# Kernel optimization log

Hardware: AMD Instinct MI355X
Metric: run time of the kernel (lower is better)

## Reference

```python
import jax, jax.numpy as jnp
import numpy as np

N = 200000
D = 256
B = 512  # fixed num_segments (batch.max()+1 in the torch code)
LN_EPS = 1e-5


def _layernorm(h, gamma, beta):
    mu = jnp.mean(h, axis=-1, keepdims=True)
    var = jnp.var(h, axis=-1, keepdims=True)
    return (h - mu) * jax.lax.rsqrt(var + LN_EPS) * gamma + beta


def setup_inputs() -> dict:
    key = jax.random.key(0)
    ks = jax.random.split(key, 10)
    x = jax.random.normal(ks[0], (N, D), dtype=jnp.float32)
    batch = jnp.sort(jax.random.randint(ks[1], (N,), 0, B)).astype(jnp.int64)
    s = 0.05
    return {
        "x": x,
        "batch": batch,
        "vn_embed": jax.random.normal(ks[2], (1, D), dtype=jnp.float32) * 0.02,
        "W1": jax.random.normal(ks[3], (D, D), dtype=jnp.float32) * s,
        "b1": jnp.zeros((D,), dtype=jnp.float32),
        "g1": jnp.ones((D,), dtype=jnp.float32),
        "be1": jnp.zeros((D,), dtype=jnp.float32),
        "W2": jax.random.normal(ks[4], (D, D), dtype=jnp.float32) * s,
        "b2": jnp.zeros((D,), dtype=jnp.float32),
        "g2": jnp.ones((D,), dtype=jnp.float32),
        "be2": jnp.zeros((D,), dtype=jnp.float32),
        "Wg": jax.random.normal(ks[5], (2 * D, D), dtype=jnp.float32) * s,
        "bg": jnp.zeros((D,), dtype=jnp.float32),
    }


def reference(x, batch, vn_embed, W1, b1, g1, be1, W2, b2, g2, be2, Wg, bg):
    # scatter-mean: per-graph average of node features  [B, D]
    seg_sum = jax.ops.segment_sum(x, batch, num_segments=B)
    cnt = jax.ops.segment_sum(jnp.ones((x.shape[0],), x.dtype), batch, num_segments=B)
    node_agg = seg_sum / jnp.maximum(cnt, 1.0)[:, None]
    # node_to_vn: Linear + GELU(exact) + LayerNorm (dropout = identity at eval)
    vn_update = _layernorm(jax.nn.gelu(node_agg @ W1 + b1, approximate=False), g1, be1)
    vn_state = vn_embed + vn_update  # vn_embed broadcasts [1,D] -> [B,D]
    # gather broadcast back to nodes + vn_to_node MLP
    vn_broadcast = vn_state[batch]  # [N, D]
    node_update = _layernorm(jax.nn.gelu(vn_broadcast @ W2 + b2, approximate=False), g2, be2)
    # sigmoid gate on concat + gated residual
    gate = jax.nn.sigmoid(jnp.concatenate([x, node_update], axis=-1) @ Wg + bg)
    x_out = x + gate * node_update
    return (x_out, vn_state)
```

## Files before the change

kernel.cpp:

```cpp
#include <hip/hip_runtime.h>
#include <hip/hip_bf16.h>
#include <math.h>

#define DIM 256
#define B_SEG 512
#define LN_EPS 1e-5f

typedef __attribute__((ext_vector_type(8))) short bf16x8;
typedef __attribute__((ext_vector_type(4))) float f32x4;

__device__ __forceinline__ float gelu_exact(float v) {
    return 0.5f * v * (1.0f + erff(v * 0.70710678118654752f));
}

__device__ __forceinline__ unsigned int pack2bf(float a, float b) {
    unsigned int ua = (unsigned int)__bfloat16_as_ushort(__float2bfloat16(a));
    unsigned int ub = (unsigned int)__bfloat16_as_ushort(__float2bfloat16(b));
    return ua | (ub << 16);
}

__device__ __forceinline__ void async16(const void* g, void* l) {
    __builtin_amdgcn_global_load_lds(
        (const __attribute__((address_space(1))) void*)(g),
        (__attribute__((address_space(3))) void*)(l), 16, 0, 0);
}

__global__ __launch_bounds__(256) void k_wprep(const float* __restrict__ Wg,
                                               __hip_bfloat16* __restrict__ Wt2) {
    int k = blockIdx.x;
    int c = threadIdx.x;
    Wt2[((size_t)(k >> 3) << 11) + (c << 3) + (k & 7)] = __float2bfloat16(Wg[(size_t)k * DIM + c]);
}

__global__ __launch_bounds__(256) void k_bounds(const int* __restrict__ batch,
                                                int* __restrict__ seg_start, int n) {
    int s = blockIdx.x * 256 + threadIdx.x;
    if (s > B_SEG) return;
    int lo = 0, hi = n;
    while (lo < hi) {
        int mid = (lo + hi) >> 1;
        if (batch[mid] < s) lo = mid + 1; else hi = mid;
    }
    seg_start[s] = lo;
}

__global__ __launch_bounds__(256) void k_segsum2(const float* __restrict__ x,
                                                 const int* __restrict__ seg_start,
                                                 float* __restrict__ partial,
                                                 __hip_bfloat16* __restrict__ xbf,
                                                 int emit) {
    const int seg  = blockIdx.x >> 1;
    const int half = blockIdx.x & 1;
    const int s0 = seg_start[seg], s1 = seg_start[seg + 1];
    const int hl = (s1 - s0 + 1) >> 1;
    const int rs = s0 + half * hl;
    const int re = half ? s1 : (s0 + hl);

    const int wave = threadIdx.x >> 6;
    const int lane = threadIdx.x & 63;
    const int dby  = lane * 8;

    float4 acc = make_float4(0.f, 0.f, 0.f, 0.f);

    for (int r0 = rs; r0 < re; r0 += 16) {
        float4 v[4];
        #pragma unroll
        for (int jj = 0; jj < 4; ++jj) {
            int r = r0 + 4 * jj + wave;
            v[jj] = (r < re) ? *(const float4*)(x + (size_t)r * DIM + lane * 4)
                             : make_float4(0.f, 0.f, 0.f, 0.f);
        }
        __builtin_amdgcn_sched_barrier(0);
        #pragma unroll
        for (int jj = 0; jj < 4; ++jj) {
            int r = r0 + 4 * jj + wave;
            if (r < re) {
                if (emit) {
                    uint2 pk;
                    pk.x = pack2bf(v[jj].x, v[jj].y);
                    pk.y = pack2bf(v[jj].z, v[jj].w);
                    *(uint2*)((char*)xbf + (size_t)r * 512 + (dby ^ ((r & 7) << 4))) = pk;
                }
                acc.x += v[jj].x; acc.y += v[jj].y; acc.z += v[jj].z; acc.w += v[jj].w;
            }
        }
    }

    __shared__ float4 red[4][64];
    red[wave][lane] = acc;
    __syncthreads();
    if (wave == 0) {
        float4 a0 = red[0][lane], a1 = red[1][lane], a2 = red[2][lane], a3 = red[3][lane];
        float4 t;
        t.x = (a0.x + a1.x) + (a2.x + a3.x);
        t.y = (a0.y + a1.y) + (a2.y + a3.y);
        t.z = (a0.z + a1.z) + (a2.z + a3.z);
        t.w = (a0.w + a1.w) + (a2.w + a3.w);
        *(float4*)(partial + ((size_t)half * B_SEG + seg) * DIM + lane * 4) = t;
    }
}

__global__ __launch_bounds__(256) void k_vn(const float* __restrict__ partial,
                                            const int* __restrict__ seg_start,
                                            const float* __restrict__ vn_embed,
                                            const float* __restrict__ W1, const float* __restrict__ b1,
                                            const float* __restrict__ g1, const float* __restrict__ be1,
                                            const float* __restrict__ W2, const float* __restrict__ b2,
                                            const float* __restrict__ g2, const float* __restrict__ be2,
                                            const float* __restrict__ Wg, const float* __restrict__ bg,
                                            float* __restrict__ vn_state_out,
                                            float* __restrict__ nu,
                                            float* __restrict__ gpart) {
    __shared__ float sIn[DIM];
    __shared__ float sRed[DIM];
    __shared__ float sRed2[DIM];
    const int b = blockIdx.x;
    const int d = threadIdx.x;

    float cntf = (float)(seg_start[b + 1] - seg_start[b]);
    float denom = fmaxf(cntf, 1.0f);
    sIn[d] = (partial[(size_t)b * DIM + d] +
              partial[(size_t)(B_SEG + b) * DIM + d]) / denom;
    __syncthreads();

    float h0 = 0.f, h1 = 0.f, h2a = 0.f, h3 = 0.f;
    for (int k = 0; k < DIM; k += 4) {
        h0  = fmaf(sIn[k + 0], W1[(size_t)(k + 0) * DIM + d], h0);
        h1  = fmaf(sIn[k + 1], W1[(size_t)(k + 1) * DIM + d], h1);
        h2a = fmaf(sIn[k + 2], W1[(size_t)(k + 2) * DIM + d], h2a);
        h3  = fmaf(sIn[k + 3], W1[(size_t)(k + 3) * DIM + d], h3);
    }
    float h = gelu_exact(b1[d] + ((h0 + h1) + (h2a + h3)));

    sRed[d] = h; sRed2[d] = h * h;
    __syncthreads();
    for (int s = 128; s > 0; s >>= 1) {
        if (d < s) { sRed[d] += sRed[d + s]; sRed2[d] += sRed2[d + s]; }
        __syncthreads();
    }
    float mu = sRed[0] * (1.0f / DIM);
    float var = fmaxf(sRed2[0] * (1.0f / DIM) - mu * mu, 0.0f);
    float rs = rsqrtf(var + LN_EPS);
    float vnst = vn_embed[d] + ((h - mu) * rs * g1[d] + be1[d]);
    vn_state_out[(size_t)b * DIM + d] = vnst;
    __syncthreads();
    sIn[d] = vnst;
    __syncthreads();

    float g0 = 0.f, g1a = 0.f, g2a = 0.f, g3 = 0.f;
    for (int k = 0; k < DIM; k += 4) {
        g0  = fmaf(sIn[k + 0], W2[(size_t)(k + 0) * DIM + d], g0);
        g1a = fmaf(sIn[k + 1], W2[(size_t)(k + 1) * DIM + d], g1a);
        g2a = fmaf(sIn[k + 2], W2[(size_t)(k + 2) * DIM + d], g2a);
        g3  = fmaf(sIn[k + 3], W2[(size_t)(k + 3) * DIM + d], g3);
    }
    float h2 = gelu_exact(b2[d] + ((g0 + g1a) + (g2a + g3)));

    sRed[d] = h2; sRed2[d] = h2 * h2;
    __syncthreads();
    for (int s = 128; s > 0; s >>= 1) {
        if (d < s) { sRed[d] += sRed[d + s]; sRed2[d] += sRed2[d + s]; }
        __syncthreads();
    }
    float mu2 = sRed[0] * (1.0f / DIM);
    float var2 = fmaxf(sRed2[0] * (1.0f / DIM) - mu2 * mu2, 0.0f);
    float rs2 = rsqrtf(var2 + LN_EPS);
    float nud = (h2 - mu2) * rs2 * g2[d] + be2[d];
    nu[(size_t)b * DIM + d] = nud;
    __syncthreads();
    sIn[d] = nud;
    __syncthreads();

    float p0 = 0.f, p1 = 0.f, p2 = 0.f, p3 = 0.f;
    for (int k = 0; k < DIM; k += 4) {
        p0 = fmaf(sIn[k + 0], Wg[(size_t)(DIM + k + 0) * DIM + d], p0);
        p1 = fmaf(sIn[k + 1], Wg[(size_t)(DIM + k + 1) * DIM + d], p1);
        p2 = fmaf(sIn[k + 2], Wg[(size_t)(DIM + k + 2) * DIM + d], p2);
        p3 = fmaf(sIn[k + 3], Wg[(size_t)(DIM + k + 3) * DIM + d], p3);
    }
    gpart[(size_t)b * DIM + d] = bg[d] + ((p0 + p1) + (p2 + p3));
}

__global__ __launch_bounds__(256, 4) void k_gate_bf(const __hip_bfloat16* __restrict__ xbf,
                                                    const int* __restrict__ batch,
                                                    const __hip_bfloat16* __restrict__ Wt2,
                                                    const float* __restrict__ nu,
                                                    const float* __restrict__ gpart,
                                                    float* __restrict__ xout,
                                                    int n) {
    __shared__ __align__(16) char sA[64 * 512];

    const int tid  = threadIdx.x;
    const int wave = tid >> 6;
    const int lane = tid & 63;
    const int r15  = lane & 15;
    const int kq   = lane >> 4;
    const size_t i0 = (size_t)blockIdx.x * 64;

    const char* gsrc = (const char*)xbf + i0 * 512;
    #pragma unroll
    for (int j = 0; j < 8; ++j)
        async16(gsrc + j * 4096 + tid * 16, sA + j * 4096 + wave * 1024);
    __syncthreads();

    f32x4 acc[4][4];
    #pragma unroll
    for (int m = 0; m < 4; ++m)
        #pragma unroll
        for (int nn = 0; nn < 4; ++nn)
            acc[m][nn] = (f32x4){0.f, 0.f, 0.f, 0.f};

    #pragma unroll
    for (int ks = 0; ks < 8; ++ks) {
        bf16x8 a[4], b[4];
        #pragma unroll
        for (int nn = 0; nn < 4; ++nn) {
            int c = wave * 64 + nn * 16 + r15;
            b[nn] = *(const bf16x8*)(Wt2 + ((size_t)(ks * 4 + kq) << 11) + (c << 3));
        }
        #pragma unroll
        for (int m = 0; m < 4; ++m) {
            int r = m * 16 + r15;
            a[m] = *(const bf16x8*)(sA + r * 512 + ((ks * 64 + kq * 16) ^ ((r & 7) << 4)));
        }
        #pragma unroll
        for (int m = 0; m < 4; ++m)
            #pragma unroll
            for (int nn = 0; nn < 4; ++nn)
                acc[m][nn] = __builtin_amdgcn_mfma_f32_16x16x32_bf16(a[m], b[nn], acc[m][nn], 0, 0, 0);
    }

    #pragma unroll
    for (int m = 0; m < 4; ++m) {
        #pragma unroll
        for (int q = 0; q < 4; ++q) {
            int rr = m * 16 + kq * 4 + q;
            long node = (long)(i0 + rr);
            if (node >= n) continue;
            int bb = batch[node];
            #pragma unroll
            for (int nn = 0; nn < 4; ++nn) {
                int col = wave * 64 + nn * 16 + r15;
                float pre = acc[m][nn][q] + gpart[bb * DIM + col];
                float e = __expf(-pre);
                float gte = __builtin_amdgcn_rcpf(1.0f + e);
                float xres = __bfloat162float(
                    *(const __hip_bfloat16*)(sA + rr * 512 + ((2 * col) ^ ((rr & 7) << 4))));
                xout[(size_t)node * DIM + col] = xres + gte * nu[bb * DIM + col];
            }
        }
    }
}

__global__ __launch_bounds__(256) void k_segsum_fp(const float* __restrict__ x,
                                                   const int* __restrict__ batch,
                                                   float* __restrict__ sums,
                                                   int n) {
    const int i0 = blockIdx.x * 64;
    if (i0 >= n) return;
    const int t    = threadIdx.x;
    const int lane = t & 63;
    const int d4   = lane * 4;
    const int rg   = t >> 6;
    float4 acc = make_float4(0.f, 0.f, 0.f, 0.f);
    int cur = -1;
    for (int j = 0; j < 16; ++j) {
        int i = i0 + rg + 4 * j;
        if (i >= n) break;
        int b = batch[i];
        if (b != cur) {
            if (cur >= 0) {
                atomicAdd(&sums[(size_t)cur * DIM + d4 + 0], acc.x);
                atomicAdd(&sums[(size_t)cur * DIM + d4 + 1], acc.y);
                atomicAdd(&sums[(size_t)cur * DIM + d4 + 2], acc.z);
                atomicAdd(&sums[(size_t)cur * DIM + d4 + 3], acc.w);
            }
            acc = make_float4(0.f, 0.f, 0.f, 0.f);
            cur = b;
        }
        float4 v = *(const float4*)(x + (size_t)i * DIM + d4);
        acc.x += v.x; acc.y += v.y; acc.z += v.z; acc.w += v.w;
    }
    if (cur >= 0) {
        atomicAdd(&sums[(size_t)cur * DIM + d4 + 0], acc.x);
        atomicAdd(&sums[(size_t)cur * DIM + d4 + 1], acc.y);
        atomicAdd(&sums[(size_t)cur * DIM + d4 + 2], acc.z);
        atomicAdd(&sums[(size_t)cur * DIM + d4 + 3], acc.w);
    }
}

__global__ __launch_bounds__(256) void k_gate_fp(const float* __restrict__ x,
                                                 const int* __restrict__ batch,
                                                 const __hip_bfloat16* __restrict__ Wt2,
                                                 const float* __restrict__ nu,
                                                 const float* __restrict__ gpart,
                                                 float* __restrict__ xout,
                                                 int n) {
    __shared__ __align__(16) char sA[32 * 512];
    const int tid  = threadIdx.x;
    const int wave = tid >> 6;
    const int lane = tid & 63;
    const int r15  = lane & 15;
    const int kq   = lane >> 4;
    const int i0   = blockIdx.x * 32;

    float4 av0[4], av1[4];
    #pragma unroll
    for (int j = 0; j < 4; ++j) {
        int v = j * 256 + tid;
        int r = v >> 5;
        int k8 = v & 31;
        int node = i0 + r;
        if (node < n) {
            const float* p = x + (size_t)node * DIM + k8 * 8;
            av0[j] = *(const float4*)p;
            av1[j] = *(const float4*)(p + 4);
        } else {
            av0[j] = make_float4(0.f, 0.f, 0.f, 0.f);
            av1[j] = av0[j];
        }
    }
    #pragma unroll
    for (int j = 0; j < 4; ++j) {
        int v = j * 256 + tid;
        int r = v >> 5;
        int k8 = v & 31;
        uint4 pk;
        pk.x = pack2bf(av0[j].x, av0[j].y);
        pk.y = pack2bf(av0[j].z, av0[j].w);
        pk.z = pack2bf(av1[j].x, av1[j].y);
        pk.w = pack2bf(av1[j].z, av1[j].w);
        *(uint4*)(sA + r * 512 + ((k8 * 16) ^ ((r & 7) << 4))) = pk;
    }
    __syncthreads();

    f32x4 acc[2][4];
    #pragma unroll
    for (int m = 0; m < 2; ++m)
        #pragma unroll
        for (int nn = 0; nn < 4; ++nn)
            acc[m][nn] = (f32x4){0.f, 0.f, 0.f, 0.f};

    #pragma unroll
    for (int ks = 0; ks < 8; ++ks) {
        bf16x8 a[2], b[4];
        #pragma unroll
        for (int nn = 0; nn < 4; ++nn) {
            int c = wave * 64 + nn * 16 + r15;
            b[nn] = *(const bf16x8*)(Wt2 + ((size_t)(ks * 4 + kq) << 11) + (c << 3));
        }
        #pragma unroll
        for (int m = 0; m < 2; ++m) {
            int r = m * 16 + r15;
            a[m] = *(const bf16x8*)(sA + r * 512 + ((ks * 64 + kq * 16) ^ ((r & 7) << 4)));
        }
        #pragma unroll
        for (int m = 0; m < 2; ++m)
            #pragma unroll
            for (int nn = 0; nn < 4; ++nn)
                acc[m][nn] = __builtin_amdgcn_mfma_f32_16x16x32_bf16(a[m], b[nn], acc[m][nn], 0, 0, 0);
    }

    #pragma unroll
    for (int m = 0; m < 2; ++m) {
        #pragma unroll
        for (int q = 0; q < 4; ++q) {
            int rr = m * 16 + kq * 4 + q;
            int node = i0 + rr;
            if (node >= n) continue;
            int bb = batch[node];
            #pragma unroll
            for (int nn = 0; nn < 4; ++nn) {
                int col = wave * 64 + nn * 16 + r15;
                float pre = acc[m][nn][q] + gpart[bb * DIM + col];
                float e = __expf(-pre);
                float gte = __builtin_amdgcn_rcpf(1.0f + e);
                float xres = __bfloat162float(
                    *(const __hip_bfloat16*)(sA + rr * 512 + ((2 * col) ^ ((rr & 7) << 4))));
                xout[(size_t)node * DIM + col] = xres + gte * nu[bb * DIM + col];
            }
        }
    }
}

extern "C" void kernel_launch(void* const* d_in, const int* in_sizes, int n_in,
                              void* d_out, int out_size, void* d_ws, size_t ws_size,
                              hipStream_t stream) {
    const float* x        = (const float*)d_in[0];
    const int*   batch    = (const int*)d_in[1];
    const float* vn_embed = (const float*)d_in[2];
    const float* W1  = (const float*)d_in[3];
    const float* b1  = (const float*)d_in[4];
    const float* g1  = (const float*)d_in[5];
    const float* be1 = (const float*)d_in[6];
    const float* W2  = (const float*)d_in[7];
    const float* b2  = (const float*)d_in[8];
    const float* g2  = (const float*)d_in[9];
    const float* be2 = (const float*)d_in[10];
    const float* Wg  = (const float*)d_in[11];
    const float* bg  = (const float*)d_in[12];

    const int n = in_sizes[0] / DIM;

    float* out = (float*)d_out;
    float* xout = out;
    float* vn_state_out = out + (size_t)n * DIM;

    char* wsb = (char*)d_ws;
    int*   seg_start = (int*)wsb;
    float* partial   = (float*)(wsb + 4096);
    float* nu        = partial + (size_t)2 * B_SEG * DIM;
    float* gpart     = nu + (size_t)B_SEG * DIM;
    __hip_bfloat16* Wt2 = (__hip_bfloat16*)(gpart + (size_t)B_SEG * DIM);
    __hip_bfloat16* xbf = Wt2 + (size_t)DIM * DIM;

    const int nt64 = (n + 63) / 64;
    const size_t base_bytes = 4096 + (size_t)2 * B_SEG * DIM * 4
                            + (size_t)B_SEG * DIM * 4 * 2 + (size_t)DIM * DIM * 2;
    const size_t need = base_bytes + (size_t)nt64 * 64 * 512;
    const bool use_bf = (ws_size >= need);

    k_wprep<<<DIM, DIM, 0, stream>>>(Wg, Wt2);
    k_bounds<<<3, 256, 0, stream>>>(batch, seg_start, n);

    if (use_bf) {
        k_segsum2<<<2 * B_SEG, 256, 0, stream>>>(x, seg_start, partial, xbf, 1);
    } else {
        hipMemsetAsync(partial, 0, (size_t)2 * B_SEG * DIM * sizeof(float), stream);
        k_segsum_fp<<<nt64, 256, 0, stream>>>(x, batch, partial, n);
    }

    k_vn<<<B_SEG, 256, 0, stream>>>(partial, seg_start, vn_embed,
                                    W1, b1, g1, be1,
                                    W2, b2, g2, be2,
                                    Wg, bg,
                                    vn_state_out, nu, gpart);

    if (use_bf) {
        k_gate_bf<<<nt64, 256, 0, stream>>>(xbf, batch, Wt2, nu, gpart, xout, n);
    } else {
        int nblk3 = (n + 31) / 32;
        k_gate_fp<<<nblk3, 256, 0, stream>>>(x, batch, Wt2, nu, gpart, xout, n);
    }
}
```

Before: 197.2 us.

## Replace per-segment segsum with per-tile partials plus boundary headers

The segment-sum pass now works on 64-row tiles instead of two blocks per segment. Each tile accumulates its first and last segment in registers, writes two partial rows plus a header naming those segments, and atomically adds any interior segments into an extra buffer. k_vn then gathers the tile partials that touch its segment. The Wg prep and bounds kernels are merged into one launch, and a memset of the extra buffer is added. The aim is to balance load across many more blocks, so uneven segment sizes matter less, at the cost of more metadata and reduction work in k_vn.

```diff
diff --git a/kernel.cpp b/kernel.cpp
--- a/kernel.cpp
+++ b/kernel.cpp
@@ -25,82 +25,115 @@
         (__attribute__((address_space(3))) void*)(l), 16, 0, 0);
 }
 
-__global__ __launch_bounds__(256) void k_wprep(const float* __restrict__ Wg,
-                                               __hip_bfloat16* __restrict__ Wt2) {
-    int k = blockIdx.x;
-    int c = threadIdx.x;
-    Wt2[((size_t)(k >> 3) << 11) + (c << 3) + (k & 7)] = __float2bfloat16(Wg[(size_t)k * DIM + c]);
-}
-
-__global__ __launch_bounds__(256) void k_bounds(const int* __restrict__ batch,
-                                                int* __restrict__ seg_start, int n) {
-    int s = blockIdx.x * 256 + threadIdx.x;
-    if (s > B_SEG) return;
-    int lo = 0, hi = n;
-    while (lo < hi) {
-        int mid = (lo + hi) >> 1;
-        if (batch[mid] < s) lo = mid + 1; else hi = mid;
-    }
-    seg_start[s] = lo;
-}
-
-__global__ __launch_bounds__(256) void k_segsum2(const float* __restrict__ x,
-                                                 const int* __restrict__ seg_start,
-                                                 float* __restrict__ partial,
-                                                 __hip_bfloat16* __restrict__ xbf,
-                                                 int emit) {
-    const int seg  = blockIdx.x >> 1;
-    const int half = blockIdx.x & 1;
-    const int s0 = seg_start[seg], s1 = seg_start[seg + 1];
-    const int hl = (s1 - s0 + 1) >> 1;
-    const int rs = s0 + half * hl;
-    const int re = half ? s1 : (s0 + hl);
+__global__ __launch_bounds__(256) void k_prep(const float* __restrict__ Wg,
+                                              __hip_bfloat16* __restrict__ Wt2,
+                                              const int* __restrict__ batch,
+                                              int* __restrict__ seg_start, int n) {
+    if (blockIdx.x < 256) {
+        int k = blockIdx.x;
+        int c = threadIdx.x;
+        Wt2[((size_t)(k >> 3) << 11) + (c << 3) + (k & 7)] = __float2bfloat16(Wg[(size_t)k * DIM + c]);
+        return;
+    }
+    for (int s = threadIdx.x; s <= B_SEG; s += 256) {
+        int lo = 0, hi = n;
+        while (lo < hi) {
+            int mid = (lo + hi) >> 1;
+            if (batch[mid] < s) lo = mid + 1; else hi = mid;
+        }
+        seg_start[s] = lo;
+    }
+}
+
+__global__ __launch_bounds__(256) void k_pass1(const float* __restrict__ x,
+                                               const int* __restrict__ batch,
+                                               float* __restrict__ part,
+                                               unsigned int* __restrict__ hdr,
+                                               float* __restrict__ extra,
+                                               __hip_bfloat16* __restrict__ xbf,
+                                               int n, int emit) {
+    const int tile = blockIdx.x;
+    const int i0   = tile * 64;
+    if (i0 >= n) return;
+    const int iN   = min(i0 + 64, n);
 
     const int wave = threadIdx.x >> 6;
     const int lane = threadIdx.x & 63;
+    const int d4   = lane * 4;
     const int dby  = lane * 8;
 
-    float4 acc = make_float4(0.f, 0.f, 0.f, 0.f);
-
-    for (int r0 = rs; r0 < re; r0 += 16) {
+    const int sf = batch[i0];
+    const int sl = batch[iN - 1];
+
+    float4 accA = make_float4(0.f, 0.f, 0.f, 0.f);
+    float4 accB = make_float4(0.f, 0.f, 0.f, 0.f);
+
+    #pragma unroll
+    for (int g = 0; g < 4; ++g) {
+        int   bt[4];
         float4 v[4];
         #pragma unroll
         for (int jj = 0; jj < 4; ++jj) {
-            int r = r0 + 4 * jj + wave;
-            v[jj] = (r < re) ? *(const float4*)(x + (size_t)r * DIM + lane * 4)
+            int r = i0 + g * 16 + 4 * jj + wave;
+            bt[jj] = (r < iN) ? batch[r] : -2;
+        }
+        #pragma unroll
+        for (int jj = 0; jj < 4; ++jj) {
+            int r = i0 + g * 16 + 4 * jj + wave;
+            v[jj] = (r < iN) ? *(const float4*)(x + (size_t)r * DIM + d4)
                              : make_float4(0.f, 0.f, 0.f, 0.f);
         }
         __builtin_amdgcn_sched_barrier(0);
         #pragma unroll
         for (int jj = 0; jj < 4; ++jj) {
-            int r = r0 + 4 * jj + wave;
-            if (r < re) {
-                if (emit) {
-                    uint2 pk;
-                    pk.x = pack2bf(v[jj].x, v[jj].y);
-                    pk.y = pack2bf(v[jj].z, v[jj].w);
-                    *(uint2*)((char*)xbf + (size_t)r * 512 + (dby ^ ((r & 7) << 4))) = pk;
-                }
-                acc.x += v[jj].x; acc.y += v[jj].y; acc.z += v[jj].z; acc.w += v[jj].w;
+            int r = i0 + g * 16 + 4 * jj + wave;
+            if (emit && r < iN) {
+                uint2 pk;
+                pk.x = pack2bf(v[jj].x, v[jj].y);
+                pk.y = pack2bf(v[jj].z, v[jj].w);
+                *(uint2*)((char*)xbf + (size_t)r * 512 + (dby ^ ((r & 7) << 4))) = pk;
             }
-        }
-    }
-
-    __shared__ float4 red[4][64];
-    red[wave][lane] = acc;
+            if (bt[jj] == sf) {
+                accA.x += v[jj].x; accA.y += v[jj].y; accA.z += v[jj].z; accA.w += v[jj].w;
+            } else if (bt[jj] == sl) {
+                accB.x += v[jj].x; accB.y += v[jj].y; accB.z += v[jj].z; accB.w += v[jj].w;
+            } else if (r < iN) {
+                atomicAdd(&extra[(size_t)bt[jj] * DIM + d4 + 0], v[jj].x);
+                atomicAdd(&extra[(size_t)bt[jj] * DIM + d4 + 1], v[jj].y);
+                atomicAdd(&extra[(size_t)bt[jj] * DIM + d4 + 2], v[jj].z);
+                atomicAdd(&extra[(size_t)bt[jj] * DIM + d4 + 3], v[jj].w);
+            }
+        }
+    }
+
+    __shared__ float4 redA[4][64];
+    __shared__ float4 redB[4][64];
+    redA[wave][lane] = accA;
+    redB[wave][lane] = accB;
     __syncthreads();
     if (wave == 0) {
-        float4 a0 = red[0][lane], a1 = red[1][lane], a2 = red[2][lane], a3 = red[3][lane];
+        float4 a0 = redA[0][lane], a1 = redA[1][lane], a2 = redA[2][lane], a3 = redA[3][lane];
         float4 t;
         t.x = (a0.x + a1.x) + (a2.x + a3.x);
         t.y = (a0.y + a1.y) + (a2.y + a3.y);
         t.z = (a0.z + a1.z) + (a2.z + a3.z);
         t.w = (a0.w + a1.w) + (a2.w + a3.w);
-        *(float4*)(partial + ((size_t)half * B_SEG + seg) * DIM + lane * 4) = t;
-    }
-}
-
-__global__ __launch_bounds__(256) void k_vn(const float* __restrict__ partial,
+        *(float4*)(part + ((size_t)tile * 2 + 0) * DIM + d4) = t;
+        if (lane == 0) hdr[tile] = (unsigned int)sf | ((unsigned int)sl << 16);
+    } else if (wave == 1) {
+        float4 a0 = redB[0][lane], a1 = redB[1][lane], a2 = redB[2][lane], a3 = redB[3][lane];
+        float4 t;
+        t.x = (a0.x + a1.x) + (a2.x + a3.x);
+        t.y = (a0.y + a1.y) + (a2.y + a3.y);
+        t.z = (a0.z + a1.z) + (a2.z + a3.z);
+        t.w = (a0.w + a1.w) + (a2.w + a3.w);
+        *(float4*)(part + ((size_t)tile * 2 + 1) * DIM + d4) = t;
+    }
+}
+
+__global__ __launch_bounds__(256) void k_vn(const float* __restrict__ part,
+                                            const unsigned int* __restrict__ hdr,
+                                            const float* __restrict__ extra,
                                             const int* __restrict__ seg_start,
                                             const float* __restrict__ vn_embed,
                                             const float* __restrict__ W1, const float* __restrict__ b1,
@@ -110,17 +143,27 @@
                                             const float* __restrict__ Wg, const float* __restrict__ bg,
                                             float* __restrict__ vn_state_out,
                                             float* __restrict__ nu,
-                                            float* __restrict__ gpart) {
+                                            float* __restrict__ gpart,
+                                            int use_parts) {
     __shared__ float sIn[DIM];
     __shared__ float sRed[DIM];
     __shared__ float sRed2[DIM];
     const int b = blockIdx.x;
     const int d = threadIdx.x;
 
-    float cntf = (float)(seg_start[b + 1] - seg_start[b]);
-    float denom = fmaxf(cntf, 1.0f);
-    sIn[d] = (partial[(size_t)b * DIM + d] +
-              partial[(size_t)(B_SEG + b) * DIM + d]) / denom;
+    const int s0 = seg_start[b], s1 = seg_start[b + 1];
+    float sum = extra[(size_t)b * DIM + d];
+    if (use_parts && s1 > s0) {
+        int t0 = s0 >> 6, t1 = (s1 - 1) >> 6;
+        for (int t = t0; t <= t1; ++t) {
+            unsigned int h = hdr[t];
+            int f = (int)(h & 0xffffu), l = (int)(h >> 16);
+            if (f == b) sum += part[((size_t)t * 2 + 0) * DIM + d];
+            if (l == b && l != f) sum += part[((size_t)t * 2 + 1) * DIM + d];
+        }
+    }
+    float denom = fmaxf((float)(s1 - s0), 1.0f);
+    sIn[d] = sum / denom;
     __syncthreads();
 
     float h0 = 0.f, h1 = 0.f, h2a = 0.f, h3 = 0.f;
@@ -401,40 +444,43 @@
     const float* bg  = (const float*)d_in[12];
 
     const int n = in_sizes[0] / DIM;
+    const int nt64 = (n + 63) / 64;
 
     float* out = (float*)d_out;
     float* xout = out;
     float* vn_state_out = out + (size_t)n * DIM;
 
     char* wsb = (char*)d_ws;
-    int*   seg_start = (int*)wsb;
-    float* partial   = (float*)(wsb + 4096);
-    float* nu        = partial + (size_t)2 * B_SEG * DIM;
-    float* gpart     = nu + (size_t)B_SEG * DIM;
+    int*          seg_start = (int*)wsb;
+    unsigned int* hdr       = (unsigned int*)(wsb + 4096);
+    float*        extra     = (float*)(wsb + 20480);
+    float*        part      = (float*)(wsb + 544768);
+    char*         after     = wsb + 544768 + (size_t)nt64 * 2 * DIM * 4;
+    float* nu    = (float*)after;
+    float* gpart = nu + (size_t)B_SEG * DIM;
     __hip_bfloat16* Wt2 = (__hip_bfloat16*)(gpart + (size_t)B_SEG * DIM);
     __hip_bfloat16* xbf = Wt2 + (size_t)DIM * DIM;
 
-    const int nt64 = (n + 63) / 64;
-    const size_t base_bytes = 4096 + (size_t)2 * B_SEG * DIM * 4
-                            + (size_t)B_SEG * DIM * 4 * 2 + (size_t)DIM * DIM * 2;
-    const size_t need = base_bytes + (size_t)nt64 * 64 * 512;
+    const size_t xbf_off = (size_t)((char*)xbf - wsb);
+    const size_t need = xbf_off + (size_t)nt64 * 64 * 512;
     const bool use_bf = (ws_size >= need);
 
-    k_wprep<<<DIM, DIM, 0, stream>>>(Wg, Wt2);
-    k_bounds<<<3, 256, 0, stream>>>(batch, seg_start, n);
+    hipMemsetAsync(extra, 0, (size_t)B_SEG * DIM * sizeof(float), stream);
+
+    k_prep<<<257, 256, 0, stream>>>(Wg, Wt2, batch, seg_start, n);
 
     if (use_bf) {
-        k_segsum2<<<2 * B_SEG, 256, 0, stream>>>(x, seg_start, partial, xbf, 1);
+        k_pass1<<<nt64, 256, 0, stream>>>(x, batch, part, hdr, extra, xbf, n, 1);
     } else {
-        hipMemsetAsync(partial, 0, (size_t)2 * B_SEG * DIM * sizeof(float), stream);
-        k_segsum_fp<<<nt64, 256, 0, stream>>>(x, batch, partial, n);
-    }
-
-    k_vn<<<B_SEG, 256, 0, stream>>>(partial, seg_start, vn_embed,
+        k_segsum_fp<<<nt64, 256, 0, stream>>>(x, batch, extra, n);
+    }
+
+    k_vn<<<B_SEG, 256, 0, stream>>>(part, hdr, extra, seg_start, vn_embed,
                                     W1, b1, g1, be1,
                                     W2, b2, g2, be2,
                                     Wg, bg,
-                                    vn_state_out, nu, gpart);
+                                    vn_state_out, nu, gpart,
+                                    use_bf ? 1 : 0);
 
     if (use_bf) {
         k_gate_bf<<<nt64, 256, 0, stream>>>(xbf, batch, Wt2, nu, gpart, xout, n);
```

After: 200.3 us. Within noise of the previous version (+1.5%).

## Split segment-sum from bf16 conversion and compute means from bf16 inside k_vn

Applied to the files above, without the earlier changes.

Merges the weight-prep, segment-bounds and workspace-zeroing kernels into a single k_prep launch. Replaces the per-segment sum kernel (one block per segment half) with a flat, load-balanced fp32-to-bf16 conversion kernel, and moves the segment-sum reduction into k_vn, which now reads the smaller bf16 copy. This is meant to cut launch count and the tail imbalance from uneven segment sizes. In exchange, the segment means are accumulated from bf16-rounded values, which lowers their precision, and k_vn takes on a serial reduction per segment.

```diff
diff --git a/kernel.cpp b/kernel.cpp
--- a/kernel.cpp
+++ b/kernel.cpp
@@ -19,88 +19,80 @@
     return ua | (ub << 16);
 }
 
+__device__ __forceinline__ float bf2f(short s) {
+    return __uint_as_float(((unsigned int)(unsigned short)s) << 16);
+}
+
 __device__ __forceinline__ void async16(const void* g, void* l) {
     __builtin_amdgcn_global_load_lds(
         (const __attribute__((address_space(1))) void*)(g),
         (__attribute__((address_space(3))) void*)(l), 16, 0, 0);
 }
 
-__global__ __launch_bounds__(256) void k_wprep(const float* __restrict__ Wg,
-                                               __hip_bfloat16* __restrict__ Wt2) {
-    int k = blockIdx.x;
-    int c = threadIdx.x;
-    Wt2[((size_t)(k >> 3) << 11) + (c << 3) + (k & 7)] = __float2bfloat16(Wg[(size_t)k * DIM + c]);
-}
-
-__global__ __launch_bounds__(256) void k_bounds(const int* __restrict__ batch,
-                                                int* __restrict__ seg_start, int n) {
-    int s = blockIdx.x * 256 + threadIdx.x;
-    if (s > B_SEG) return;
-    int lo = 0, hi = n;
-    while (lo < hi) {
-        int mid = (lo + hi) >> 1;
-        if (batch[mid] < s) lo = mid + 1; else hi = mid;
-    }
-    seg_start[s] = lo;
-}
-
-__global__ __launch_bounds__(256) void k_segsum2(const float* __restrict__ x,
-                                                 const int* __restrict__ seg_start,
-                                                 float* __restrict__ partial,
+__global__ __launch_bounds__(256) void k_prep(const float* __restrict__ Wg,
+                                              __hip_bfloat16* __restrict__ Wt2,
+                                              const int* __restrict__ batch,
+                                              int* __restrict__ seg_start,
+                                              float* __restrict__ extra, int n) {
+    if (blockIdx.x < 256) {
+        int k = blockIdx.x;
+        int c = threadIdx.x;
+        Wt2[((size_t)(k >> 3) << 11) + (c << 3) + (k & 7)] = __float2bfloat16(Wg[(size_t)k * DIM + c]);
+        return;
+    }
+    if (blockIdx.x == 256) {
+        for (int s = threadIdx.x; s <= B_SEG; s += 256) {
+            int lo = 0, hi = n;
+            while (lo < hi) {
+                int mid = (lo + hi) >> 1;
+                if (batch[mid] < s) lo = mid + 1; else hi = mid;
+            }
+            seg_start[s] = lo;
+        }
+        return;
+    }
+    int b = blockIdx.x - 257;
+    ((float4*)extra)[(size_t)b * 256 + threadIdx.x] = make_float4(0.f, 0.f, 0.f, 0.f);
+}
+
+__global__ __launch_bounds__(256) void k_convert(const float* __restrict__ x,
                                                  __hip_bfloat16* __restrict__ xbf,
-                                                 int emit) {
-    const int seg  = blockIdx.x >> 1;
-    const int half = blockIdx.x & 1;
-    const int s0 = seg_start[seg], s1 = seg_start[seg + 1];
-    const int hl = (s1 - s0 + 1) >> 1;
-    const int rs = s0 + half * hl;
-    const int re = half ? s1 : (s0 + hl);
-
-    const int wave = threadIdx.x >> 6;
-    const int lane = threadIdx.x & 63;
-    const int dby  = lane * 8;
-
-    float4 acc = make_float4(0.f, 0.f, 0.f, 0.f);
-
-    for (int r0 = rs; r0 < re; r0 += 16) {
-        float4 v[4];
-        #pragma unroll
-        for (int jj = 0; jj < 4; ++jj) {
-            int r = r0 + 4 * jj + wave;
-            v[jj] = (r < re) ? *(const float4*)(x + (size_t)r * DIM + lane * 4)
-                             : make_float4(0.f, 0.f, 0.f, 0.f);
-        }
-        __builtin_amdgcn_sched_barrier(0);
-        #pragma unroll
-        for (int jj = 0; jj < 4; ++jj) {
-            int r = r0 + 4 * jj + wave;
-            if (r < re) {
-                if (emit) {
-                    uint2 pk;
-                    pk.x = pack2bf(v[jj].x, v[jj].y);
-                    pk.y = pack2bf(v[jj].z, v[jj].w);
-                    *(uint2*)((char*)xbf + (size_t)r * 512 + (dby ^ ((r & 7) << 4))) = pk;
-                }
-                acc.x += v[jj].x; acc.y += v[jj].y; acc.z += v[jj].z; acc.w += v[jj].w;
-            }
-        }
-    }
-
-    __shared__ float4 red[4][64];
-    red[wave][lane] = acc;
-    __syncthreads();
-    if (wave == 0) {
-        float4 a0 = red[0][lane], a1 = red[1][lane], a2 = red[2][lane], a3 = red[3][lane];
-        float4 t;
-        t.x = (a0.x + a1.x) + (a2.x + a3.x);
-        t.y = (a0.y + a1.y) + (a2.y + a3.y);
-        t.z = (a0.z + a1.z) + (a2.z + a3.z);
-        t.w = (a0.w + a1.w) + (a2.w + a3.w);
-        *(float4*)(partial + ((size_t)half * B_SEG + seg) * DIM + lane * 4) = t;
-    }
-}
-
-__global__ __launch_bounds__(256) void k_vn(const float* __restrict__ partial,
+                                                 size_t chunks) {
+    const size_t base   = (size_t)blockIdx.x * 256 + threadIdx.x;
+    const size_t stride = (size_t)gridDim.x * 256;
+
+    float4 v0[8], v1[8];
+    #pragma unroll
+    for (int j = 0; j < 8; ++j) {
+        size_t g = base + (size_t)j * stride;
+        if (g < chunks) {
+            size_t r = g >> 5;
+            int    c = (int)(g & 31);
+            const float4* p = (const float4*)(x + r * DIM + c * 8);
+            v0[j] = p[0];
+            v1[j] = p[1];
+        } else {
+            v0[j] = make_float4(0.f, 0.f, 0.f, 0.f);
+            v1[j] = v0[j];
+        }
+    }
+    __builtin_amdgcn_sched_barrier(0);
+    #pragma unroll
+    for (int j = 0; j < 8; ++j) {
+        size_t g = base + (size_t)j * stride;
+        if (g < chunks) {
+            size_t r = g >> 5;
+            int    c = (int)(g & 31);
+            uint4 pk;
+            pk.x = pack2bf(v0[j].x, v0[j].y); pk.y = pack2bf(v0[j].z, v0[j].w);
+            pk.z = pack2bf(v1[j].x, v1[j].y); pk.w = pack2bf(v1[j].z, v1[j].w);
+            *(uint4*)((char*)xbf + r * 512 + ((c * 16) ^ ((int)(r & 7) << 4))) = pk;
+        }
+    }
+}
+
+__global__ __launch_bounds__(256) void k_vn(const __hip_bfloat16* __restrict__ xbf,
+                                            const float* __restrict__ extra,
                                             const int* __restrict__ seg_start,
                                             const float* __restrict__ vn_embed,
                                             const float* __restrict__ W1, const float* __restrict__ b1,
@@ -110,17 +102,39 @@
                                             const float* __restrict__ Wg, const float* __restrict__ bg,
                                             float* __restrict__ vn_state_out,
                                             float* __restrict__ nu,
-                                            float* __restrict__ gpart) {
+                                            float* __restrict__ gpart,
+                                            int use_bf) {
     __shared__ float sIn[DIM];
     __shared__ float sRed[DIM];
     __shared__ float sRed2[DIM];
+    __shared__ float sG[8 * DIM];
     const int b = blockIdx.x;
     const int d = threadIdx.x;
 
-    float cntf = (float)(seg_start[b + 1] - seg_start[b]);
-    float denom = fmaxf(cntf, 1.0f);
-    sIn[d] = (partial[(size_t)b * DIM + d] +
-              partial[(size_t)(B_SEG + b) * DIM + d]) / denom;
+    const int s0 = seg_start[b], s1 = seg_start[b + 1];
+    float sum;
+    if (use_bf) {
+        const int h  = threadIdx.x >> 5;
+        const int li = threadIdx.x & 31;
+        float acc[8] = {0.f, 0.f, 0.f, 0.f, 0.f, 0.f, 0.f, 0.f};
+        for (int r = s0 + h; r < s1; r += 8) {
+            bf16x8 w = *(const bf16x8*)((const char*)xbf + (size_t)r * 512 +
+                                        ((li * 16) ^ ((r & 7) << 4)));
+            #pragma unroll
+            for (int e = 0; e < 8; ++e) acc[e] += bf2f(w[e]);
+        }
+        #pragma unroll
+        for (int e = 0; e < 8; ++e) sG[h * DIM + li * 8 + e] = acc[e];
+        __syncthreads();
+        float s = 0.f;
+        #pragma unroll
+        for (int h2 = 0; h2 < 8; ++h2) s += sG[h2 * DIM + d];
+        sum = s;
+    } else {
+        sum = extra[(size_t)b * DIM + d];
+    }
+    float denom = fmaxf((float)(s1 - s0), 1.0f);
+    sIn[d] = sum / denom;
     __syncthreads();
 
     float h0 = 0.f, h1 = 0.f, h2a = 0.f, h3 = 0.f;
@@ -401,6 +415,7 @@
     const float* bg  = (const float*)d_in[12];
 
     const int n = in_sizes[0] / DIM;
+    const int nt64 = (n + 63) / 64;
 
     float* out = (float*)d_out;
     float* xout = out;
@@ -408,33 +423,32 @@
 
     char* wsb = (char*)d_ws;
     int*   seg_start = (int*)wsb;
-    float* partial   = (float*)(wsb + 4096);
-    float* nu        = partial + (size_t)2 * B_SEG * DIM;
+    float* extra     = (float*)(wsb + 4096);
+    float* nu        = extra + (size_t)B_SEG * DIM;
     float* gpart     = nu + (size_t)B_SEG * DIM;
     __hip_bfloat16* Wt2 = (__hip_bfloat16*)(gpart + (size_t)B_SEG * DIM);
     __hip_bfloat16* xbf = Wt2 + (size_t)DIM * DIM;
 
-    const int nt64 = (n + 63) / 64;
-    const size_t base_bytes = 4096 + (size_t)2 * B_SEG * DIM * 4
-                            + (size_t)B_SEG * DIM * 4 * 2 + (size_t)DIM * DIM * 2;
-    const size_t need = base_bytes + (size_t)nt64 * 64 * 512;
+    const size_t xbf_off = (size_t)((char*)xbf - wsb);
+    const size_t need = xbf_off + (size_t)nt64 * 64 * 512;
     const bool use_bf = (ws_size >= need);
 
-    k_wprep<<<DIM, DIM, 0, stream>>>(Wg, Wt2);
-    k_bounds<<<3, 256, 0, stream>>>(batch, seg_start, n);
+    k_prep<<<385, 256, 0, stream>>>(Wg, Wt2, batch, seg_start, extra, n);
 
     if (use_bf) {
-        k_segsum2<<<2 * B_SEG, 256, 0, stream>>>(x, seg_start, partial, xbf, 1);
+        const size_t chunks = (size_t)n * 32;
+        int cblk = (int)((chunks + 2047) / 2048);
+        k_convert<<<cblk, 256, 0, stream>>>(x, xbf, chunks);
     } else {
-        hipMemsetAsync(partial, 0, (size_t)2 * B_SEG * DIM * sizeof(float), stream);
-        k_segsum_fp<<<nt64, 256, 0, stream>>>(x, batch, partial, n);
-    }
-
-    k_vn<<<B_SEG, 256, 0, stream>>>(partial, seg_start, vn_embed,
+        k_segsum_fp<<<nt64, 256, 0, stream>>>(x, batch, extra, n);
+    }
+
+    k_vn<<<B_SEG, 256, 0, stream>>>(xbf, extra, seg_start, vn_embed,
                                     W1, b1, g1, be1,
                                     W2, b2, g2, be2,
                                     Wg, bg,
-                                    vn_state_out, nu, gpart);
+                                    vn_state_out, nu, gpart,
+                                    use_bf ? 1 : 0);
 
     if (use_bf) {
         k_gate_bf<<<nt64, 256, 0, stream>>>(xbf, batch, Wt2, nu, gpart, xout, n);
```

After: 205.2 us. 4.0% more time.
